# Optimization experiments

Measured on AMD Instinct MI355X. Metric: run time of the kernel, lower is better.

## Reference

```python
import jax, jax.numpy as jnp
import numpy as np

WS = 8
NUM_HEADS = 16
DIM = 256
BN_EPS = 1e-5

def _relative_position_index(ws):
    coords = np.stack(np.meshgrid(np.arange(ws), np.arange(ws), indexing='ij'))  # (2, ws, ws)
    flat = coords.reshape(2, -1)                      # (2, N)
    rel = flat[:, :, None] - flat[:, None, :]          # (2, N, N)
    rel = rel.transpose(1, 2, 0).copy()                # (N, N, 2)
    rel[:, :, 0] += ws - 1
    rel[:, :, 1] += ws - 1
    rel[:, :, 0] *= 2 * ws - 1
    return rel.sum(-1)                                 # (N, N) int

REL_IDX = jnp.asarray(_relative_position_index(WS))

def setup_inputs() -> dict:
    key = jax.random.key(0)
    ks = jax.random.split(key, 7)
    B, C, H, W = 2, DIM, 192, 192
    x = jax.random.normal(ks[0], (B, C, H, W), dtype=jnp.float32)
    w_qk = jax.random.normal(ks[1], (2 * C, C), dtype=jnp.float32) * 0.05  # 1x1 conv kernel
    gamma = 1.0 + 0.1 * jax.random.normal(ks[2], (2 * C,), dtype=jnp.float32)
    beta = 0.1 * jax.random.normal(ks[3], (2 * C,), dtype=jnp.float32)
    rmean = 0.1 * jax.random.normal(ks[4], (2 * C,), dtype=jnp.float32)
    rvar = jax.random.uniform(ks[5], (2 * C,), dtype=jnp.float32, minval=0.5, maxval=1.5)
    rel_table = 0.02 * jax.random.normal(ks[6], ((2 * WS - 1) ** 2, NUM_HEADS), dtype=jnp.float32)
    return {"x": x, "w_qk": w_qk, "gamma": gamma, "beta": beta,
            "rmean": rmean, "rvar": rvar, "rel_table": rel_table}

def reference(x, w_qk, gamma, beta, rmean, rvar, rel_table):
    B, C, H, W = x.shape
    h = NUM_HEADS
    d = C // h
    scale = d ** -0.5
    ws = WS
    N = ws * ws
    hh, ww = H // ws, W // ws
    # 1x1 conv -> BN (eval: running stats) -> ReLU
    qk = jnp.einsum('bchw,oc->bohw', x, w_qk)
    inv = gamma / jnp.sqrt(rvar + BN_EPS)
    qk = qk * inv[None, :, None, None] + (beta - rmean * inv)[None, :, None, None]
    qk = jax.nn.relu(qk)
    # rearrange 'b (qkv h d) (hh ws1) (ww ws2) -> qkv (b hh ww) h (ws1 ws2) d'
    qk = qk.reshape(B, 2, h, d, hh, ws, ww, ws)
    qk = qk.transpose(1, 0, 4, 6, 2, 5, 7, 3).reshape(2, B * hh * ww, h, N, d)
    q, k = qk[0], qk[1]
    dots = jnp.einsum('whnd,whmd->whnm', q, k) * scale  # (Bn, h, N, N)
    bias = rel_table[REL_IDX.reshape(-1)].reshape(N, N, h).transpose(2, 0, 1)
    dots = dots + bias[None]
    # avgpool over heads, then over query tokens -> (Bn, N, 1)
    avg = dots.mean(axis=1).mean(axis=1)[:, :, None]
    attn = jax.nn.softmax(dots, axis=-1)
    return attn, avg
```

## Files before the change

kernel.cpp:

```cpp
#include <hip/hip_runtime.h>
#include <hip/hip_bf16.h>

typedef __bf16 bf16;
typedef __bf16 bf16x4 __attribute__((ext_vector_type(4)));
typedef __bf16 bf16x8 __attribute__((ext_vector_type(8)));
typedef float f32x4 __attribute__((ext_vector_type(4)));

#define WS_INV 262144
#define WS_ADD 264192
#define WS_BIAS 266240

#define XS_STRIDE 264
#define QK_STRIDE 520
#define LDS_AVG_OFF 66560
#define LDS_STG_OFF 68608
#define STG_STRIDE 68
#define LDS_BYTES (68608 + 8704)

__global__ void prep_kernel(const float* __restrict__ w_qk,
                            const float* __restrict__ gamma,
                            const float* __restrict__ beta,
                            const float* __restrict__ rmean,
                            const float* __restrict__ rvar,
                            const float* __restrict__ rel_table,
                            char* __restrict__ ws) {
  bf16* wbf = (bf16*)ws;
  float* invb = (float*)(ws + WS_INV);
  float* addb = (float*)(ws + WS_ADD);
  float* biasb = (float*)(ws + WS_BIAS);
  int bid = blockIdx.x, t = threadIdx.x;
  if (bid < 512) {
    int o = bid;
    wbf[o * 256 + t] = (bf16)w_qk[o * 256 + t];
    if (t == 0) {
      float iv = gamma[o] * rsqrtf(rvar[o] + 1e-5f);
      invb[o] = iv;
      addb[o] = beta[o] - rmean[o] * iv;
    }
  } else {
    int base = (bid - 512) * 1024 + t * 4;
#pragma unroll
    for (int i = 0; i < 4; ++i) {
      int flat = base + i;
      int h = flat >> 12, n = (flat >> 6) & 63, m = flat & 63;
      int idx = ((n >> 3) - (m >> 3) + 7) * 15 + ((n & 7) - (m & 7) + 7);
      biasb[flat] = rel_table[idx * 16 + h];
    }
  }
}

__global__ __launch_bounds__(512)
void fused_kernel(const float* __restrict__ x, const char* __restrict__ ws,
                  float* __restrict__ out_attn, float* __restrict__ out_avg) {
  const bf16* __restrict__ wbf = (const bf16*)ws;
  const float* __restrict__ invb = (const float*)(ws + WS_INV);
  const float* __restrict__ addb = (const float*)(ws + WS_ADD);
  const float* __restrict__ biasb = (const float*)(ws + WS_BIAS);

  __shared__ __attribute__((aligned(16))) char smem[LDS_BYTES];
  bf16* xs = (bf16*)smem;
  bf16* qk = (bf16*)smem;
  float* avgp = (float*)(smem + LDS_AVG_OFF);

  const int bid = blockIdx.x;
  const int win = (bid & 7) * 144 + (bid >> 3);
  const int b = win / 576;
  const int rem = win - b * 576;
  const int wy = rem / 24, wx = rem - (rem / 24) * 24;

  const int tid = threadIdx.x;
  const int w = tid >> 6;
  const int l = tid & 63;
  const int lg = l >> 4;
  const int ll = l & 15;

  float* stgw = (float*)(smem + LDS_STG_OFF) + w * (4 * STG_STRIDE);

  {
    const float* xb = x + (size_t)b * 256 * 36864 + (size_t)(wy * 8) * 192 + wx * 8;
    const int c = tid & 255;
    const int half = tid >> 8;
#pragma unroll
    for (int p = 0; p < 4; ++p) {
      int ws1 = p * 2 + half;
      const float* src = xb + (size_t)c * 36864 + ws1 * 192;
      float4 v0 = *(const float4*)src;
      float4 v1 = *(const float4*)(src + 4);
      bf16* dst = xs + (ws1 * 8) * XS_STRIDE + c;
      dst[0 * XS_STRIDE] = (bf16)v0.x;
      dst[1 * XS_STRIDE] = (bf16)v0.y;
      dst[2 * XS_STRIDE] = (bf16)v0.z;
      dst[3 * XS_STRIDE] = (bf16)v0.w;
      dst[4 * XS_STRIDE] = (bf16)v1.x;
      dst[5 * XS_STRIDE] = (bf16)v1.y;
      dst[6 * XS_STRIDE] = (bf16)v1.z;
      dst[7 * XS_STRIDE] = (bf16)v1.w;
    }
  }
  __syncthreads();

  f32x4 acc[4][4];
#pragma unroll
  for (int mt = 0; mt < 4; ++mt)
#pragma unroll
    for (int nt = 0; nt < 4; ++nt)
      acc[mt][nt] = (f32x4){0.f, 0.f, 0.f, 0.f};

  const int obase = w * 64;
  for (int kk = 0; kk < 8; ++kk) {
    bf16x8 a[4], bb[4];
#pragma unroll
    for (int mt = 0; mt < 4; ++mt)
      a[mt] = *(const bf16x8*)(wbf + (size_t)(obase + mt * 16 + ll) * 256 + kk * 32 + lg * 8);
#pragma unroll
    for (int nt = 0; nt < 4; ++nt)
      bb[nt] = *(const bf16x8*)(xs + (nt * 16 + ll) * XS_STRIDE + kk * 32 + lg * 8);
#pragma unroll
    for (int mt = 0; mt < 4; ++mt)
#pragma unroll
      for (int nt = 0; nt < 4; ++nt)
        acc[mt][nt] = __builtin_amdgcn_mfma_f32_16x16x32_bf16(a[mt], bb[nt], acc[mt][nt], 0, 0, 0);
  }
  __syncthreads();

#pragma unroll
  for (int mt = 0; mt < 4; ++mt) {
    const int ob = obase + mt * 16 + lg * 4;
    float iv0 = invb[ob + 0], iv1 = invb[ob + 1], iv2 = invb[ob + 2], iv3 = invb[ob + 3];
    float ad0 = addb[ob + 0], ad1 = addb[ob + 1], ad2 = addb[ob + 2], ad3 = addb[ob + 3];
#pragma unroll
    for (int nt = 0; nt < 4; ++nt) {
      int px = nt * 16 + ll;
      bf16x4 pack;
      pack[0] = (bf16)fmaxf(acc[mt][nt][0] * iv0 + ad0, 0.f);
      pack[1] = (bf16)fmaxf(acc[mt][nt][1] * iv1 + ad1, 0.f);
      pack[2] = (bf16)fmaxf(acc[mt][nt][2] * iv2 + ad2, 0.f);
      pack[3] = (bf16)fmaxf(acc[mt][nt][3] * iv3 + ad3, 0.f);
      *(bf16x4*)(qk + px * QK_STRIDE + ob) = pack;
    }
  }
  __syncthreads();

  bf16x8 zfrag;
#pragma unroll
  for (int i = 0; i < 8; ++i) zfrag[i] = (bf16)0.f;

  float psum[4] = {0.f, 0.f, 0.f, 0.f};

  for (int hh = 0; hh < 2; ++hh) {
    const int h = w * 2 + hh;
    bf16x8 qa[4];
#pragma unroll
    for (int nt = 0; nt < 4; ++nt) {
      bf16x8 v = *(const bf16x8*)(qk + (nt * 16 + ll) * QK_STRIDE + h * 16 + (lg & 1) * 8);
      qa[nt] = (l < 32) ? v : zfrag;
    }
    f32x4 s[4][4];
#pragma unroll
    for (int mt = 0; mt < 4; ++mt) {
      bf16x8 kb = *(const bf16x8*)(qk + (mt * 16 + ll) * QK_STRIDE + 256 + h * 16 + (lg & 1) * 8);
      kb = (l < 32) ? kb : zfrag;
#pragma unroll
      for (int nt = 0; nt < 4; ++nt) {
        f32x4 z = {0.f, 0.f, 0.f, 0.f};
        s[nt][mt] = __builtin_amdgcn_mfma_f32_16x16x32_bf16(qa[nt], kb, z, 0, 0, 0);
      }
    }
    const float* bh = biasb + h * 4096;
#pragma unroll
    for (int nt = 0; nt < 4; ++nt) {
#pragma unroll
      for (int j = 0; j < 4; ++j) {
        int n = nt * 16 + lg * 4 + j;
#pragma unroll
        for (int mt = 0; mt < 4; ++mt) {
          float v = s[nt][mt][j] * 0.25f + bh[n * 64 + mt * 16 + ll];
          s[nt][mt][j] = v;
          psum[mt] += v;
        }
      }
    }
#pragma unroll
    for (int nt = 0; nt < 4; ++nt) {
#pragma unroll
      for (int j = 0; j < 4; ++j) {
        float mx = fmaxf(fmaxf(s[nt][0][j], s[nt][1][j]), fmaxf(s[nt][2][j], s[nt][3][j]));
        mx = fmaxf(mx, __shfl_xor(mx, 1));
        mx = fmaxf(mx, __shfl_xor(mx, 2));
        mx = fmaxf(mx, __shfl_xor(mx, 4));
        mx = fmaxf(mx, __shfl_xor(mx, 8));
        float sum = 0.f;
#pragma unroll
        for (int mt = 0; mt < 4; ++mt) {
          float e = __expf(s[nt][mt][j] - mx);
          s[nt][mt][j] = e;
          sum += e;
        }
        sum += __shfl_xor(sum, 1);
        sum += __shfl_xor(sum, 2);
        sum += __shfl_xor(sum, 4);
        sum += __shfl_xor(sum, 8);
        float rinv = __builtin_amdgcn_rcpf(sum);
#pragma unroll
        for (int mt = 0; mt < 4; ++mt)
          stgw[lg * STG_STRIDE + mt * 16 + ll] = s[nt][mt][j] * rinv;
        f32x4 v = *(const f32x4*)(stgw + lg * STG_STRIDE + 4 * ll);
        int n = nt * 16 + lg * 4 + j;
        *(f32x4*)(out_attn + ((size_t)(win * 16 + h) * 64 + n) * 64 + 4 * ll) = v;
      }
    }
  }

#pragma unroll
  for (int mt = 0; mt < 4; ++mt) {
    psum[mt] += __shfl_xor(psum[mt], 16);
    psum[mt] += __shfl_xor(psum[mt], 32);
  }
  if (l < 16) {
#pragma unroll
    for (int mt = 0; mt < 4; ++mt)
      avgp[w * 64 + mt * 16 + l] = psum[mt];
  }
  __syncthreads();
  if (tid < 64) {
    float t = 0.f;
#pragma unroll
    for (int w2 = 0; w2 < 8; ++w2) t += avgp[w2 * 64 + tid];
    out_avg[win * 64 + tid] = t * (1.f / 1024.f);
  }
}

extern "C" void kernel_launch(void* const* d_in, const int* in_sizes, int n_in,
                              void* d_out, int out_size, void* d_ws, size_t ws_size,
                              hipStream_t stream) {
  const float* x     = (const float*)d_in[0];
  const float* w_qk  = (const float*)d_in[1];
  const float* gamma = (const float*)d_in[2];
  const float* beta  = (const float*)d_in[3];
  const float* rmean = (const float*)d_in[4];
  const float* rvar  = (const float*)d_in[5];
  const float* rel   = (const float*)d_in[6];
  float* out = (float*)d_out;
  char* ws = (char*)d_ws;

  prep_kernel<<<576, 256, 0, stream>>>(w_qk, gamma, beta, rmean, rvar, rel, ws);
  fused_kernel<<<1152, 512, 0, stream>>>(x, ws, out, out + (size_t)75497472);
}
```

Before: 451.7 us.

## Split fused kernel into separate GEMM and attention kernels via workspace

```diff
diff --git a/kernel.cpp b/kernel.cpp
--- a/kernel.cpp
+++ b/kernel.cpp
@@ -9,13 +9,16 @@
 #define WS_INV 262144
 #define WS_ADD 264192
 #define WS_BIAS 266240
+#define WS_QKT 1048576
 
 #define XS_STRIDE 264
 #define QK_STRIDE 520
+#define QK_WIN_BYTES 66560
+
 #define LDS_AVG_OFF 66560
 #define LDS_STG_OFF 68608
 #define STG_STRIDE 68
-#define LDS_BYTES (68608 + 8704)
+#define LDS_B_BYTES (68608 + 8704)
 
 __global__ void prep_kernel(const float* __restrict__ w_qk,
                             const float* __restrict__ gamma,
@@ -50,17 +53,15 @@
 }
 
 __global__ __launch_bounds__(512)
-void fused_kernel(const float* __restrict__ x, const char* __restrict__ ws,
-                  float* __restrict__ out_attn, float* __restrict__ out_avg) {
+void gemm_kernel(const float* __restrict__ x, char* __restrict__ ws) {
   const bf16* __restrict__ wbf = (const bf16*)ws;
   const float* __restrict__ invb = (const float*)(ws + WS_INV);
   const float* __restrict__ addb = (const float*)(ws + WS_ADD);
-  const float* __restrict__ biasb = (const float*)(ws + WS_BIAS);
-
-  __shared__ __attribute__((aligned(16))) char smem[LDS_BYTES];
+  bf16* __restrict__ qkt = (bf16*)(ws + WS_QKT);
+
+  __shared__ __attribute__((aligned(16))) char smem[QK_WIN_BYTES];
   bf16* xs = (bf16*)smem;
   bf16* qk = (bf16*)smem;
-  float* avgp = (float*)(smem + LDS_AVG_OFF);
 
   const int bid = blockIdx.x;
   const int win = (bid & 7) * 144 + (bid >> 3);
@@ -73,8 +74,6 @@
   const int l = tid & 63;
   const int lg = l >> 4;
   const int ll = l & 15;
-
-  float* stgw = (float*)(smem + LDS_STG_OFF) + w * (4 * STG_STRIDE);
 
   {
     const float* xb = x + (size_t)b * 256 * 36864 + (size_t)(wy * 8) * 192 + wx * 8;
@@ -141,6 +140,55 @@
   }
   __syncthreads();
 
+  {
+    char* dst = (char*)(qkt) + (size_t)win * QK_WIN_BYTES;
+#pragma unroll
+    for (int it = 0; it < 8; ++it) {
+      int byte = (it * 512 + tid) * 16;
+      *(f32x4*)(dst + byte) = *(const f32x4*)(smem + byte);
+    }
+    if (tid < 64) {
+      int byte = 65536 + tid * 16;
+      *(f32x4*)(dst + byte) = *(const f32x4*)(smem + byte);
+    }
+  }
+}
+
+__global__ __launch_bounds__(512, 4)
+void attn_kernel(const char* __restrict__ ws,
+                 float* __restrict__ out_attn, float* __restrict__ out_avg) {
+  const float* __restrict__ biasb = (const float*)(ws + WS_BIAS);
+  const bf16* __restrict__ qkt = (const bf16*)(ws + WS_QKT);
+
+  __shared__ __attribute__((aligned(16))) char smem[LDS_B_BYTES];
+  bf16* qk = (bf16*)smem;
+  float* avgp = (float*)(smem + LDS_AVG_OFF);
+
+  const int bid = blockIdx.x;
+  const int win = (bid & 7) * 144 + (bid >> 3);
+
+  const int tid = threadIdx.x;
+  const int w = tid >> 6;
+  const int l = tid & 63;
+  const int lg = l >> 4;
+  const int ll = l & 15;
+
+  float* stgw = (float*)(smem + LDS_STG_OFF) + w * (4 * STG_STRIDE);
+
+  {
+    const char* src = (const char*)(qkt) + (size_t)win * QK_WIN_BYTES;
+#pragma unroll
+    for (int it = 0; it < 8; ++it) {
+      int byte = (it * 512 + tid) * 16;
+      *(f32x4*)(smem + byte) = *(const f32x4*)(src + byte);
+    }
+    if (tid < 64) {
+      int byte = 65536 + tid * 16;
+      *(f32x4*)(smem + byte) = *(const f32x4*)(src + byte);
+    }
+  }
+  __syncthreads();
+
   bf16x8 zfrag;
 #pragma unroll
   for (int i = 0; i < 8; ++i) zfrag[i] = (bf16)0.f;
@@ -244,5 +292,6 @@
   char* ws = (char*)d_ws;
 
   prep_kernel<<<576, 256, 0, stream>>>(w_qk, gamma, beta, rmean, rvar, rel, ws);
-  fused_kernel<<<1152, 512, 0, stream>>>(x, ws, out, out + (size_t)75497472);
-}
+  gemm_kernel<<<1152, 512, 0, stream>>>(x, ws);
+  attn_kernel<<<1152, 512, 0, stream>>>(ws, out, out + (size_t)75497472);
+}
```

After: 479.0 us. 1.06x slower.

## Split fused kernel into row-tiled GEMM and per-window attention kernels

Applied to the files above, without the earlier changes.

```diff
diff --git a/kernel.cpp b/kernel.cpp
--- a/kernel.cpp
+++ b/kernel.cpp
@@ -9,13 +9,16 @@
 #define WS_INV 262144
 #define WS_ADD 264192
 #define WS_BIAS 266240
+#define WS_QKT 1048576
 
 #define XS_STRIDE 264
 #define QK_STRIDE 520
+#define QK_WIN_BYTES 65536
+
 #define LDS_AVG_OFF 66560
 #define LDS_STG_OFF 68608
 #define STG_STRIDE 68
-#define LDS_BYTES (68608 + 8704)
+#define LDS_B_BYTES (68608 + 8704)
 
 __global__ void prep_kernel(const float* __restrict__ w_qk,
                             const float* __restrict__ gamma,
@@ -50,23 +53,20 @@
 }
 
 __global__ __launch_bounds__(512)
-void fused_kernel(const float* __restrict__ x, const char* __restrict__ ws,
-                  float* __restrict__ out_attn, float* __restrict__ out_avg) {
+void gemm_kernel(const float* __restrict__ x, char* __restrict__ ws) {
   const bf16* __restrict__ wbf = (const bf16*)ws;
   const float* __restrict__ invb = (const float*)(ws + WS_INV);
   const float* __restrict__ addb = (const float*)(ws + WS_ADD);
-  const float* __restrict__ biasb = (const float*)(ws + WS_BIAS);
-
-  __shared__ __attribute__((aligned(16))) char smem[LDS_BYTES];
+  bf16* __restrict__ qkt = (bf16*)(ws + WS_QKT);
+
+  __shared__ __attribute__((aligned(16))) char smem[64 * XS_STRIDE * 2];
   bf16* xs = (bf16*)smem;
-  bf16* qk = (bf16*)smem;
-  float* avgp = (float*)(smem + LDS_AVG_OFF);
-
-  const int bid = blockIdx.x;
-  const int win = (bid & 7) * 144 + (bid >> 3);
-  const int b = win / 576;
-  const int rem = win - b * 576;
-  const int wy = rem / 24, wx = rem - (rem / 24) * 24;
+
+  const int tile = blockIdx.x;
+  const int b = tile / 576;
+  const int r = tile - b * 576;
+  const int h = r / 3;
+  const int third = r - h * 3;
 
   const int tid = threadIdx.x;
   const int w = tid >> 6;
@@ -74,27 +74,18 @@
   const int lg = l >> 4;
   const int ll = l & 15;
 
-  float* stgw = (float*)(smem + LDS_STG_OFF) + w * (4 * STG_STRIDE);
-
   {
-    const float* xb = x + (size_t)b * 256 * 36864 + (size_t)(wy * 8) * 192 + wx * 8;
-    const int c = tid & 255;
-    const int half = tid >> 8;
-#pragma unroll
-    for (int p = 0; p < 4; ++p) {
-      int ws1 = p * 2 + half;
-      const float* src = xb + (size_t)c * 36864 + ws1 * 192;
-      float4 v0 = *(const float4*)src;
-      float4 v1 = *(const float4*)(src + 4);
-      bf16* dst = xs + (ws1 * 8) * XS_STRIDE + c;
-      dst[0 * XS_STRIDE] = (bf16)v0.x;
-      dst[1 * XS_STRIDE] = (bf16)v0.y;
-      dst[2 * XS_STRIDE] = (bf16)v0.z;
-      dst[3 * XS_STRIDE] = (bf16)v0.w;
-      dst[4 * XS_STRIDE] = (bf16)v1.x;
-      dst[5 * XS_STRIDE] = (bf16)v1.y;
-      dst[6 * XS_STRIDE] = (bf16)v1.z;
-      dst[7 * XS_STRIDE] = (bf16)v1.w;
+    const float* xrow = x + (size_t)b * 256 * 36864 + h * 192 + third * 64;
+    const int cbase = tid >> 4;
+    const int px4 = (tid & 15) * 4;
+#pragma unroll
+    for (int p = 0; p < 8; ++p) {
+      int c = p * 32 + cbase;
+      float4 v = *(const float4*)(xrow + (size_t)c * 36864 + px4);
+      xs[(px4 + 0) * XS_STRIDE + c] = (bf16)v.x;
+      xs[(px4 + 1) * XS_STRIDE + c] = (bf16)v.y;
+      xs[(px4 + 2) * XS_STRIDE + c] = (bf16)v.z;
+      xs[(px4 + 3) * XS_STRIDE + c] = (bf16)v.w;
     }
   }
   __syncthreads();
@@ -121,8 +112,9 @@
       for (int nt = 0; nt < 4; ++nt)
         acc[mt][nt] = __builtin_amdgcn_mfma_f32_16x16x32_bf16(a[mt], bb[nt], acc[mt][nt], 0, 0, 0);
   }
-  __syncthreads();
-
+
+  const int winBase = b * 576 + (h >> 3) * 24 + third * 8;
+  const int pxwRow = (h & 7) * 8;
 #pragma unroll
   for (int mt = 0; mt < 4; ++mt) {
     const int ob = obase + mt * 16 + lg * 4;
@@ -131,12 +123,46 @@
 #pragma unroll
     for (int nt = 0; nt < 4; ++nt) {
       int px = nt * 16 + ll;
+      int win = winBase + (px >> 3);
+      int pxw = pxwRow + (px & 7);
       bf16x4 pack;
       pack[0] = (bf16)fmaxf(acc[mt][nt][0] * iv0 + ad0, 0.f);
       pack[1] = (bf16)fmaxf(acc[mt][nt][1] * iv1 + ad1, 0.f);
       pack[2] = (bf16)fmaxf(acc[mt][nt][2] * iv2 + ad2, 0.f);
       pack[3] = (bf16)fmaxf(acc[mt][nt][3] * iv3 + ad3, 0.f);
-      *(bf16x4*)(qk + px * QK_STRIDE + ob) = pack;
+      *(bf16x4*)(qkt + (size_t)win * 32768 + pxw * 512 + ob) = pack;
+    }
+  }
+}
+
+__global__ __launch_bounds__(512)
+void attn_kernel(const char* __restrict__ ws,
+                 float* __restrict__ out_attn, float* __restrict__ out_avg) {
+  const float* __restrict__ biasb = (const float*)(ws + WS_BIAS);
+  const char* __restrict__ qkt = ws + WS_QKT;
+
+  __shared__ __attribute__((aligned(16))) char smem[LDS_B_BYTES];
+  bf16* qk = (bf16*)smem;
+  float* avgp = (float*)(smem + LDS_AVG_OFF);
+
+  const int bid = blockIdx.x;
+  const int win = (bid & 7) * 144 + (bid >> 3);
+
+  const int tid = threadIdx.x;
+  const int w = tid >> 6;
+  const int l = tid & 63;
+  const int lg = l >> 4;
+  const int ll = l & 15;
+
+  float* stgw = (float*)(smem + LDS_STG_OFF) + w * (4 * STG_STRIDE);
+
+  {
+    const char* src = qkt + (size_t)win * QK_WIN_BYTES;
+#pragma unroll
+    for (int p = 0; p < 8; ++p) {
+      int k = p * 512 + tid;
+      int px = k >> 6, c16 = k & 63;
+      *(f32x4*)(smem + px * 1040 + c16 * 16) = *(const f32x4*)(src + (size_t)k * 16);
     }
   }
   __syncthreads();
@@ -244,5 +270,6 @@
   char* ws = (char*)d_ws;
 
   prep_kernel<<<576, 256, 0, stream>>>(w_qk, gamma, beta, rmean, rvar, rel, ws);
-  fused_kernel<<<1152, 512, 0, stream>>>(x, ws, out, out + (size_t)75497472);
-}
+  gemm_kernel<<<1152, 512, 0, stream>>>(x, ws);
+  attn_kernel<<<1152, 512, 0, stream>>>(ws, out, out + (size_t)75497472);
+}
```

Measured after the change: 478.9 us. 1.06x slower.
